# Kernel optimization log

Measured on AMD Instinct MI355X. Metric: run time of the kernel, lower is better.

Reference implementation:

```python
import jax, jax.numpy as jnp
import numpy as np

STRIDE = (1, 1)
PAD = (1, 1)
DIL = (1, 1)
GROUPS = 1
DG = 1  # deformable_groups
KH, KW = 3, 3


def setup_inputs() -> dict:
    key = jax.random.key(0)
    k1, k2, k3, k4 = jax.random.split(key, 4)
    x = jax.random.normal(k1, (8, 256, 64, 64), jnp.float32)
    offset = jax.random.normal(k2, (8, DG * 2 * KH * KW, 64, 64), jnp.float32)
    weight = jax.random.normal(k3, (256, 256, KH, KW), jnp.float32) * 0.05
    bias = jax.random.normal(k4, (256,), jnp.float32)
    return {"x": x, "offset": offset, "weight": weight, "bias": bias}


def _deform_conv2d(x, offset, weight, bias):
    N, C, H, W = x.shape
    Cout = weight.shape[0]
    Ho = (H + 2 * PAD[0] - (DIL[0] * (KH - 1) + 1)) // STRIDE[0] + 1
    Wo = (W + 2 * PAD[1] - (DIL[1] * (KW - 1) + 1)) // STRIDE[1] + 1
    K = KH * KW
    Cg = C // DG

    # offset layout: [N, DG, K, 2(y,x), Ho, Wo]
    off = offset.reshape(N, DG, K, 2, Ho, Wo)

    ky, kx = jnp.meshgrid(jnp.arange(KH), jnp.arange(KW), indexing="ij")
    ky = (ky.reshape(K) * DIL[0]).astype(jnp.float32)  # [K]
    kx = (kx.reshape(K) * DIL[1]).astype(jnp.float32)
    base_y = (jnp.arange(Ho) * STRIDE[0] - PAD[0]).astype(jnp.float32)  # [Ho]
    base_x = (jnp.arange(Wo) * STRIDE[1] - PAD[1]).astype(jnp.float32)  # [Wo]

    # sampling positions [N, DG, K, Ho, Wo]
    py = base_y[None, None, None, :, None] + ky[None, None, :, None, None] + off[:, :, :, 0]
    px = base_x[None, None, None, None, :] + kx[None, None, :, None, None] + off[:, :, :, 1]

    y0f = jnp.floor(py)
    x0f = jnp.floor(px)
    ly = py - y0f
    lx = px - x0f
    hy = 1.0 - ly
    hx = 1.0 - lx
    y0 = y0f.astype(jnp.int32)
    x0 = x0f.astype(jnp.int32)
    y1 = y0 + 1
    x1 = x0 + 1

    img = x.reshape(N, DG, Cg, H * W)

    def gather(yi, xi):
        valid = ((yi >= 0) & (yi < H) & (xi >= 0) & (xi < W)).astype(x.dtype)
        idx = jnp.clip(yi, 0, H - 1) * W + jnp.clip(xi, 0, W - 1)  # [N,DG,K,Ho,Wo]
        flat = idx.reshape(N, DG, 1, K * Ho * Wo)
        v = jnp.take_along_axis(img, flat, axis=3).reshape(N, DG, Cg, K, Ho, Wo)
        return v * valid[:, :, None]

    # bilinear combine -> columns [N, DG, Cg, K, Ho, Wo]
    cols = (
        (hy * hx)[:, :, None] * gather(y0, x0)
        + (hy * lx)[:, :, None] * gather(y0, x1)
        + (ly * hx)[:, :, None] * gather(y1, x0)
        + (ly * lx)[:, :, None] * gather(y1, x1)
    )

    # grouped conv accumulation
    P = Ho * Wo
    cols = cols.reshape(N, GROUPS, C // GROUPS, K, P)
    w = weight.reshape(GROUPS, Cout // GROUPS, C // GROUPS, K)
    out = jnp.einsum("ngckp,gock->ngop", cols, w).reshape(N, Cout, Ho, Wo)
    return out + bias[None, :, None, None]


def reference(x, offset, weight, bias):
    return _deform_conv2d(x, offset, weight, bias)
```

## Files before the change

kernel.cpp:

```cpp
#include <hip/hip_runtime.h>


#define H 64
#define W 64
#define CIN 256
#define COUT 256
#define NIMG 8
#define KTAPS 9
#define CK (CIN * KTAPS)
#define NCHUNK 72

typedef _Float16 f16;
typedef __attribute__((ext_vector_type(8))) _Float16 f16x8;
typedef __attribute__((ext_vector_type(4))) float f32x4;

__global__ __launch_bounds__(256) void dcn_wprep(const float* __restrict__ w,
                                                 f16* __restrict__ wt) {
    __shared__ f16 tw[CK];
    const int co = blockIdx.x;
    const int t = threadIdx.x;
    const float* wr = w + (size_t)co * CK + t * 9;
    float v[9];
#pragma unroll
    for (int j = 0; j < 9; ++j) v[j] = wr[j];
#pragma unroll
    for (int j = 0; j < 9; ++j) tw[j * 256 + t] = (f16)v[j];
    __syncthreads();
    f16* o = wt + (size_t)co * CK;
    for (int i = t; i < CK / 8; i += 256)
        *(f16x8*)(o + i * 8) = *(const f16x8*)(tw + i * 8);
}

__global__ __launch_bounds__(256) void dcn_xprep(const float* __restrict__ x,
                                                 f16* __restrict__ xt) {
    __shared__ f16 tl[64][66];
    const int b = blockIdx.x;
    const int n = b >> 8, pb = (b >> 2) & 63, cb = b & 3;
    const float* xn = x + (size_t)(n * CIN + cb * 64) * (H * W) + pb * 64;
    const int t = threadIdx.x;
    const int c = t >> 4;
    const int p4 = (t & 15) * 4;
#pragma unroll
    for (int pass = 0; pass < 4; ++pass) {
        float4 v = *(const float4*)(xn + (size_t)(c + pass * 16) * (H * W) + p4);
        const int cc = c + pass * 16;
        tl[p4 + 0][cc] = (f16)v.x;
        tl[p4 + 1][cc] = (f16)v.y;
        tl[p4 + 2][cc] = (f16)v.z;
        tl[p4 + 3][cc] = (f16)v.w;
    }
    __syncthreads();
    const int p = t >> 2, cq = (t & 3) * 16;
    f16* dst = xt + (size_t)n * (H * W) * CIN + (size_t)(pb * 64 + p) * CIN + cb * 64 + cq;
    *(f16x8*)dst = *(const f16x8*)&tl[p][cq];
    *(f16x8*)(dst + 8) = *(const f16x8*)&tl[p][cq + 8];
}

__global__ __launch_bounds__(256, 2) void dcn_mfma(
    const f16* __restrict__ xt, const float* __restrict__ offset,
    const f16* __restrict__ wt, const float* __restrict__ bias,
    float* __restrict__ out) {
    __shared__ int s_pix[4][KTAPS][64];
    __shared__ f16 s_wbh[4][KTAPS][64];
    __shared__ f16 s_cols[2][64][40];

    const int tid = threadIdx.x;
    const int bx = blockIdx.x;
    const int n = bx >> 6, t_img = bx & 63;
    const int tile_y = (t_img >> 3) << 3, tile_x = (t_img & 7) << 3;

    const float* offn = offset + (size_t)n * 18 * (H * W);
    for (int e = tid; e < KTAPS * 64; e += 256) {
        int k = e >> 6, p = e & 63;
        int oy = tile_y + (p >> 3), ox = tile_x + (p & 7);
        float offy = offn[(k * 2 + 0) * (H * W) + oy * W + ox];
        float offx = offn[(k * 2 + 1) * (H * W) + oy * W + ox];
        float py = (float)(oy - 1 + (k / 3)) + offy;
        float px = (float)(ox - 1 + (k % 3)) + offx;
        float y0f = floorf(py), x0f = floorf(px);
        int y0 = (int)y0f, x0 = (int)x0f, y1 = y0 + 1, x1 = x0 + 1;
        float ly = py - y0f, lx = px - x0f, hy = 1.f - ly, hx = 1.f - lx;
        bool vy0 = (y0 >= 0) && (y0 < H), vy1 = (y1 >= 0) && (y1 < H);
        bool vx0 = (x0 >= 0) && (x0 < W), vx1 = (x1 >= 0) && (x1 < W);
        int cy0 = min(max(y0, 0), H - 1), cx0 = min(max(x0, 0), W - 1);
        int cy1 = min(max(y1, 0), H - 1), cx1 = min(max(x1, 0), W - 1);
        s_pix[0][k][p] = (cy0 * W + cx0) * (CIN * 2);
        s_pix[1][k][p] = (cy0 * W + cx1) * (CIN * 2);
        s_pix[2][k][p] = (cy1 * W + cx0) * (CIN * 2);
        s_pix[3][k][p] = (cy1 * W + cx1) * (CIN * 2);
        s_wbh[0][k][p] = (f16)((vy0 && vx0) ? hy * hx : 0.f);
        s_wbh[1][k][p] = (f16)((vy0 && vx1) ? hy * lx : 0.f);
        s_wbh[2][k][p] = (f16)((vy1 && vx0) ? ly * hx : 0.f);
        s_wbh[3][k][p] = (f16)((vy1 && vx1) ? ly * lx : 0.f);
    }

    f32x4 acc[4][4];
#pragma unroll
    for (int i = 0; i < 4; ++i)
#pragma unroll
        for (int j = 0; j < 4; ++j) acc[i][j] = (f32x4)0.f;

    const int lane = tid & 63, wv = tid >> 6;
    const int co_base = wv * 64;
    const int pix_s = wv * 16 + (lane >> 2);
    const int cq16 = (lane & 3) * 16;
    const char* xb = (const char*)(xt + (size_t)n * (H * W) * CIN);

    const f16* arow[4];
#pragma unroll
    for (int cf = 0; cf < 4; ++cf)
        arow[cf] = wt + (size_t)(co_base + 16 * cf + (lane & 15)) * CK + (lane >> 4) * 8;

    __syncthreads();

    f16x8 af[4];
    {
        const char* base = xb + cq16;
        f16x8 h0 = *(const f16x8*)(base + s_pix[0][0][pix_s]);
        f16x8 h1 = *(const f16x8*)(base + s_pix[1][0][pix_s]);
        f16x8 h2 = *(const f16x8*)(base + s_pix[2][0][pix_s]);
        f16x8 h3 = *(const f16x8*)(base + s_pix[3][0][pix_s]);
#pragma unroll
        for (int cf = 0; cf < 4; ++cf) af[cf] = *(const f16x8*)(arow[cf]);
        f16x8 v = h0 * s_wbh[0][0][pix_s] + h1 * s_wbh[1][0][pix_s] +
                  h2 * s_wbh[2][0][pix_s] + h3 * s_wbh[3][0][pix_s];
        *(f16x8*)((char*)&s_cols[0][pix_s][0] + cq16) = v;
    }
    __syncthreads();

    for (int cc = 0; cc < NCHUNK; ++cc) {
        const int cur = cc & 1, nx = cur ^ 1;
        const int c1 = cc + 1;
        f16x8 h0, h1, h2, h3, afn[4];
        f16 w0, w1, w2, w3;
        if (c1 < NCHUNK) {
            const int tap = c1 >> 3;
            const char* base = xb + (c1 & 7) * 64 + cq16;
            h0 = *(const f16x8*)(base + s_pix[0][tap][pix_s]);
            h1 = *(const f16x8*)(base + s_pix[1][tap][pix_s]);
            h2 = *(const f16x8*)(base + s_pix[2][tap][pix_s]);
            h3 = *(const f16x8*)(base + s_pix[3][tap][pix_s]);
            w0 = s_wbh[0][tap][pix_s];
            w1 = s_wbh[1][tap][pix_s];
            w2 = s_wbh[2][tap][pix_s];
            w3 = s_wbh[3][tap][pix_s];
            const int k0 = c1 * 32;
#pragma unroll
            for (int cf = 0; cf < 4; ++cf) afn[cf] = *(const f16x8*)(arow[cf] + k0);
        }
        f16x8 bf[4];
#pragma unroll
        for (int pf = 0; pf < 4; ++pf)
            bf[pf] = *(const f16x8*)&s_cols[cur][16 * pf + (lane & 15)][(lane >> 4) * 8];
#pragma unroll
        for (int cf = 0; cf < 4; ++cf)
#pragma unroll
            for (int pf = 0; pf < 4; ++pf)
                acc[cf][pf] =
                    __builtin_amdgcn_mfma_f32_16x16x32_f16(af[cf], bf[pf], acc[cf][pf], 0, 0, 0);
        if (c1 < NCHUNK) {
            f16x8 v = h0 * w0 + h1 * w1 + h2 * w2 + h3 * w3;
            *(f16x8*)((char*)&s_cols[nx][pix_s][0] + cq16) = v;
#pragma unroll
            for (int cf = 0; cf < 4; ++cf) af[cf] = afn[cf];
        }
        __syncthreads();
    }

    float* outn = out + (size_t)n * COUT * (H * W);
#pragma unroll
    for (int cf = 0; cf < 4; ++cf) {
#pragma unroll
        for (int r = 0; r < 4; ++r) {
            int co = co_base + 16 * cf + ((lane >> 4) << 2) + r;
            float b = bias[co];
#pragma unroll
            for (int pf = 0; pf < 4; ++pf) {
                int pp = 16 * pf + (lane & 15);
                int oy = tile_y + (pp >> 3), ox = tile_x + (pp & 7);
                outn[(size_t)co * (H * W) + oy * W + ox] = acc[cf][pf][r] + b;
            }
        }
    }
}

__global__ __launch_bounds__(256) void dcn_transpose_w(const float* __restrict__ w,
                                                       float* __restrict__ wt) {
    __shared__ float tile[32][33];
    const int ckb = blockIdx.x * 32;
    const int cob = blockIdx.y * 32;
    const int tx = threadIdx.x & 31;
    const int ty = threadIdx.x >> 5;
#pragma unroll
    for (int i = 0; i < 32; i += 8)
        tile[ty + i][tx] = w[(size_t)(cob + ty + i) * CK + ckb + tx];
    __syncthreads();
#pragma unroll
    for (int i = 0; i < 32; i += 8)
        wt[(size_t)(ckb + ty + i) * COUT + cob + tx] = tile[tx][ty + i];
}

__global__ __launch_bounds__(256, 2) void dcn_main(
    const float* __restrict__ x, const float* __restrict__ offset,
    const float* __restrict__ wt, const float* __restrict__ bias,
    float* __restrict__ out) {
    __shared__ int s_idx[4][KTAPS][64];
    __shared__ float s_bw[4][KTAPS][64];
    __shared__ float s_W[36][COUT];
    __shared__ float s_cols[36][64];

    const int tid = threadIdx.x;
    const int bx = blockIdx.x;
    const int n = bx >> 6;
    const int t_img = bx & 63;
    const int tile_y = (t_img >> 3) << 3;
    const int tile_x = (t_img & 7) << 3;

    const float* offn = offset + (size_t)n * 18 * (H * W);
    for (int e = tid; e < KTAPS * 64; e += 256) {
        int k = e >> 6, p = e & 63;
        int oy = tile_y + (p >> 3), ox = tile_x + (p & 7);
        float offy = offn[(k * 2 + 0) * (H * W) + oy * W + ox];
        float offx = offn[(k * 2 + 1) * (H * W) + oy * W + ox];
        float py = (float)(oy - 1 + (k / 3)) + offy;
        float px = (float)(ox - 1 + (k % 3)) + offx;
        float y0f = floorf(py), x0f = floorf(px);
        int y0 = (int)y0f, x0 = (int)x0f, y1 = y0 + 1, x1 = x0 + 1;
        float ly = py - y0f, lx = px - x0f, hy = 1.f - ly, hx = 1.f - lx;
        bool vy0 = (y0 >= 0) && (y0 < H), vy1 = (y1 >= 0) && (y1 < H);
        bool vx0 = (x0 >= 0) && (x0 < W), vx1 = (x1 >= 0) && (x1 < W);
        int cy0 = min(max(y0, 0), H - 1), cx0 = min(max(x0, 0), W - 1);
        int cy1 = min(max(y1, 0), H - 1), cx1 = min(max(x1, 0), W - 1);
        s_idx[0][k][p] = cy0 * W + cx0;
        s_idx[1][k][p] = cy0 * W + cx1;
        s_idx[2][k][p] = cy1 * W + cx0;
        s_idx[3][k][p] = cy1 * W + cx1;
        s_bw[0][k][p] = (vy0 && vx0) ? hy * hx : 0.f;
        s_bw[1][k][p] = (vy0 && vx1) ? hy * lx : 0.f;
        s_bw[2][k][p] = (vy1 && vx0) ? ly * hx : 0.f;
        s_bw[3][k][p] = (vy1 && vx1) ? ly * lx : 0.f;
    }

    float acc[8][8];
#pragma unroll
    for (int i = 0; i < 8; ++i)
#pragma unroll
        for (int j = 0; j < 8; ++j) acc[i][j] = 0.f;

    const int ty = tid >> 3;
    const int tx = tid & 7;
    const int q = tid >> 6;
    const int pl = tid & 63;
    const float* xn = x + (size_t)(n * CIN) * (H * W);

    for (int ch = 0; ch < CIN / 4; ++ch) {
        const int c0 = ch * 4;
        __syncthreads();
        {
            const int rbase = q * KTAPS;
            const int co4 = (tid & 63) * 4;
#pragma unroll
            for (int i = 0; i < KTAPS; ++i) {
                int r = rbase + i;
                *reinterpret_cast<float4*>(&s_W[r][co4]) =
                    *reinterpret_cast<const float4*>(&wt[(size_t)(c0 * KTAPS + r) * COUT + co4]);
            }
        }
#pragma unroll
        for (int s = 0; s < KTAPS; ++s) {
            int r = q + 4 * s;
            int c = r / 9;
            int k = r - c * 9;
            const float* xc = xn + (size_t)(c0 + c) * (H * W);
            float v = s_bw[0][k][pl] * xc[s_idx[0][k][pl]] +
                      s_bw[1][k][pl] * xc[s_idx[1][k][pl]] +
                      s_bw[2][k][pl] * xc[s_idx[2][k][pl]] +
                      s_bw[3][k][pl] * xc[s_idx[3][k][pl]];
            s_cols[r][pl] = v;
        }
        __syncthreads();
#pragma unroll 4
        for (int r = 0; r < 36; ++r) {
            const float4 cv0 = *reinterpret_cast<const float4*>(&s_cols[r][tx * 8]);
            const float4 cv1 = *reinterpret_cast<const float4*>(&s_cols[r][tx * 8 + 4]);
            const float4 wv0 = *reinterpret_cast<const float4*>(&s_W[r][ty * 8]);
            const float4 wv1 = *reinterpret_cast<const float4*>(&s_W[r][ty * 8 + 4]);
            const float wa[8] = {wv0.x, wv0.y, wv0.z, wv0.w, wv1.x, wv1.y, wv1.z, wv1.w};
            const float ca[8] = {cv0.x, cv0.y, cv0.z, cv0.w, cv1.x, cv1.y, cv1.z, cv1.w};
#pragma unroll
            for (int i = 0; i < 8; ++i)
#pragma unroll
                for (int j = 0; j < 8; ++j) acc[i][j] += wa[i] * ca[j];
        }
    }

    float* outn = out + (size_t)(n * COUT) * (H * W);
    const int obase = (tile_y + tx) * W + tile_x;
#pragma unroll
    for (int i = 0; i < 8; ++i) {
        int co = ty * 8 + i;
        float b = bias[co];
        float4 o0, o1;
        o0.x = acc[i][0] + b; o0.y = acc[i][1] + b; o0.z = acc[i][2] + b; o0.w = acc[i][3] + b;
        o1.x = acc[i][4] + b; o1.y = acc[i][5] + b; o1.z = acc[i][6] + b; o1.w = acc[i][7] + b;
        float* po = &outn[(size_t)co * (H * W) + obase];
        *reinterpret_cast<float4*>(po) = o0;
        *reinterpret_cast<float4*>(po + 4) = o1;
    }
}

extern "C" void kernel_launch(void* const* d_in, const int* in_sizes, int n_in,
                              void* d_out, int out_size, void* d_ws, size_t ws_size,
                              hipStream_t stream) {
    const float* x = (const float*)d_in[0];
    const float* offset = (const float*)d_in[1];
    const float* weight = (const float*)d_in[2];
    const float* bias = (const float*)d_in[3];
    float* out = (float*)d_out;

    const size_t XT_OFF = 2u * 1024 * 1024;
    const size_t need = XT_OFF + (size_t)NIMG * H * W * CIN * sizeof(f16);

    if (ws_size >= need) {
        f16* wt = (f16*)d_ws;
        f16* xt = (f16*)((char*)d_ws + XT_OFF);
        dcn_wprep<<<COUT, 256, 0, stream>>>(weight, wt);
        dcn_xprep<<<NIMG * 64 * 4, 256, 0, stream>>>(x, xt);
        dcn_mfma<<<NIMG * 64, 256, 0, stream>>>(xt, offset, wt, bias, out);
    } else {
        float* wt = (float*)d_ws;
        dim3 tgrid(CK / 32, COUT / 32);
        dcn_transpose_w<<<tgrid, 256, 0, stream>>>(weight, wt);
        dcn_main<<<NIMG * 64, 256, 0, stream>>>(x, offset, wt, bias, out);
    }
}
```

Measured before the change: 185.7 us.

## Double waves per MFMA block, prefetch gathers two chunks ahead, fuse prep kernels

Merges the weight and input prep kernels into a single launch. The main MFMA kernel moves to 512 threads, so each wave covers 32 pixels instead of 64, and each thread gathers half as much data (f16x4). Bilinear gathers are now issued two chunks ahead to hide global latency. Block-to-image mapping is interleaved across images. The per-wave B-fragment reuse is halved in exchange for more waves per CU to hide gather latency; the occupancy hint of 4 blocks of 512 threads may not be reachable given register pressure.

```diff
diff --git a/kernel.cpp b/kernel.cpp
--- a/kernel.cpp
+++ b/kernel.cpp
@@ -11,52 +11,53 @@
 #define NCHUNK 72
 
 typedef _Float16 f16;
+typedef __attribute__((ext_vector_type(4))) _Float16 f16x4;
 typedef __attribute__((ext_vector_type(8))) _Float16 f16x8;
 typedef __attribute__((ext_vector_type(4))) float f32x4;
 
-__global__ __launch_bounds__(256) void dcn_wprep(const float* __restrict__ w,
-                                                 f16* __restrict__ wt) {
+__global__ __launch_bounds__(256) void dcn_prep(const float* __restrict__ x,
+                                                const float* __restrict__ w,
+                                                f16* __restrict__ xt,
+                                                f16* __restrict__ wt) {
+    __shared__ f16 tl[64][66];
     __shared__ f16 tw[CK];
-    const int co = blockIdx.x;
+    const int b = blockIdx.x;
     const int t = threadIdx.x;
-    const float* wr = w + (size_t)co * CK + t * 9;
-    float v[9];
-#pragma unroll
-    for (int j = 0; j < 9; ++j) v[j] = wr[j];
-#pragma unroll
-    for (int j = 0; j < 9; ++j) tw[j * 256 + t] = (f16)v[j];
-    __syncthreads();
-    f16* o = wt + (size_t)co * CK;
-    for (int i = t; i < CK / 8; i += 256)
-        *(f16x8*)(o + i * 8) = *(const f16x8*)(tw + i * 8);
-}
-
-__global__ __launch_bounds__(256) void dcn_xprep(const float* __restrict__ x,
-                                                 f16* __restrict__ xt) {
-    __shared__ f16 tl[64][66];
-    const int b = blockIdx.x;
-    const int n = b >> 8, pb = (b >> 2) & 63, cb = b & 3;
-    const float* xn = x + (size_t)(n * CIN + cb * 64) * (H * W) + pb * 64;
-    const int t = threadIdx.x;
-    const int c = t >> 4;
-    const int p4 = (t & 15) * 4;
-#pragma unroll
-    for (int pass = 0; pass < 4; ++pass) {
-        float4 v = *(const float4*)(xn + (size_t)(c + pass * 16) * (H * W) + p4);
-        const int cc = c + pass * 16;
-        tl[p4 + 0][cc] = (f16)v.x;
-        tl[p4 + 1][cc] = (f16)v.y;
-        tl[p4 + 2][cc] = (f16)v.z;
-        tl[p4 + 3][cc] = (f16)v.w;
-    }
-    __syncthreads();
-    const int p = t >> 2, cq = (t & 3) * 16;
-    f16* dst = xt + (size_t)n * (H * W) * CIN + (size_t)(pb * 64 + p) * CIN + cb * 64 + cq;
-    *(f16x8*)dst = *(const f16x8*)&tl[p][cq];
-    *(f16x8*)(dst + 8) = *(const f16x8*)&tl[p][cq + 8];
-}
-
-__global__ __launch_bounds__(256, 2) void dcn_mfma(
+    if (b < 2048) {
+        const int n = b >> 8, pb = (b >> 2) & 63, cb = b & 3;
+        const float* xn = x + (size_t)(n * CIN + cb * 64) * (H * W) + pb * 64;
+        const int c = t >> 4;
+        const int p4 = (t & 15) * 4;
+#pragma unroll
+        for (int pass = 0; pass < 4; ++pass) {
+            float4 v = *(const float4*)(xn + (size_t)(c + pass * 16) * (H * W) + p4);
+            const int cc = c + pass * 16;
+            tl[p4 + 0][cc] = (f16)v.x;
+            tl[p4 + 1][cc] = (f16)v.y;
+            tl[p4 + 2][cc] = (f16)v.z;
+            tl[p4 + 3][cc] = (f16)v.w;
+        }
+        __syncthreads();
+        const int p = t >> 2, cq = (t & 3) * 16;
+        f16* dst = xt + (size_t)n * (H * W) * CIN + (size_t)(pb * 64 + p) * CIN + cb * 64 + cq;
+        *(f16x8*)dst = *(const f16x8*)&tl[p][cq];
+        *(f16x8*)(dst + 8) = *(const f16x8*)&tl[p][cq + 8];
+    } else {
+        const int co = b - 2048;
+        const float* wr = w + (size_t)co * CK + t * 9;
+        float v[9];
+#pragma unroll
+        for (int j = 0; j < 9; ++j) v[j] = wr[j];
+#pragma unroll
+        for (int j = 0; j < 9; ++j) tw[j * 256 + t] = (f16)v[j];
+        __syncthreads();
+        f16* o = wt + (size_t)co * CK;
+        for (int i = t; i < CK / 8; i += 256)
+            *(f16x8*)(o + i * 8) = *(const f16x8*)(tw + i * 8);
+    }
+}
+
+__global__ __launch_bounds__(512, 4) void dcn_mfma(
     const f16* __restrict__ xt, const float* __restrict__ offset,
     const f16* __restrict__ wt, const float* __restrict__ bias,
     float* __restrict__ out) {
@@ -66,11 +67,12 @@
 
     const int tid = threadIdx.x;
     const int bx = blockIdx.x;
-    const int n = bx >> 6, t_img = bx & 63;
+    const int n = bx & 7;
+    const int t_img = bx >> 3;
     const int tile_y = (t_img >> 3) << 3, tile_x = (t_img & 7) << 3;
 
     const float* offn = offset + (size_t)n * 18 * (H * W);
-    for (int e = tid; e < KTAPS * 64; e += 256) {
+    for (int e = tid; e < KTAPS * 64; e += 512) {
         int k = e >> 6, p = e & 63;
         int oy = tile_y + (p >> 3), ox = tile_x + (p & 7);
         float offy = offn[(k * 2 + 0) * (H * W) + oy * W + ox];
@@ -94,16 +96,19 @@
         s_wbh[3][k][p] = (f16)((vy1 && vx1) ? ly * lx : 0.f);
     }
 
-    f32x4 acc[4][4];
+    f32x4 acc[4][2];
 #pragma unroll
     for (int i = 0; i < 4; ++i)
 #pragma unroll
-        for (int j = 0; j < 4; ++j) acc[i][j] = (f32x4)0.f;
+        for (int j = 0; j < 2; ++j) acc[i][j] = (f32x4)0.f;
 
     const int lane = tid & 63, wv = tid >> 6;
-    const int co_base = wv * 64;
-    const int pix_s = wv * 16 + (lane >> 2);
-    const int cq16 = (lane & 3) * 16;
+    const int wvco = wv & 3, hp = wv >> 2;
+    const int co_base = wvco * 64;
+    const int pxbase = hp * 32;
+
+    const int pix_g = tid >> 3;
+    const int poff = (tid & 7) * 8;
     const char* xb = (const char*)(xt + (size_t)n * (H * W) * CIN);
 
     const f16* arow[4];
@@ -113,54 +118,63 @@
 
     __syncthreads();
 
+    {
+        const char* base = xb + poff;
+        f16x4 g0 = *(const f16x4*)(base + s_pix[0][0][pix_g]);
+        f16x4 g1 = *(const f16x4*)(base + s_pix[1][0][pix_g]);
+        f16x4 g2 = *(const f16x4*)(base + s_pix[2][0][pix_g]);
+        f16x4 g3 = *(const f16x4*)(base + s_pix[3][0][pix_g]);
+        f16x4 v = g0 * s_wbh[0][0][pix_g] + g1 * s_wbh[1][0][pix_g] +
+                  g2 * s_wbh[2][0][pix_g] + g3 * s_wbh[3][0][pix_g];
+        *(f16x4*)((char*)&s_cols[0][pix_g][0] + poff) = v;
+    }
+    f16x4 hb0, hb1, hb2, hb3;
+    {
+        const char* base = xb + 64 + poff;
+        hb0 = *(const f16x4*)(base + s_pix[0][0][pix_g]);
+        hb1 = *(const f16x4*)(base + s_pix[1][0][pix_g]);
+        hb2 = *(const f16x4*)(base + s_pix[2][0][pix_g]);
+        hb3 = *(const f16x4*)(base + s_pix[3][0][pix_g]);
+    }
     f16x8 af[4];
-    {
-        const char* base = xb + cq16;
-        f16x8 h0 = *(const f16x8*)(base + s_pix[0][0][pix_s]);
-        f16x8 h1 = *(const f16x8*)(base + s_pix[1][0][pix_s]);
-        f16x8 h2 = *(const f16x8*)(base + s_pix[2][0][pix_s]);
-        f16x8 h3 = *(const f16x8*)(base + s_pix[3][0][pix_s]);
-#pragma unroll
-        for (int cf = 0; cf < 4; ++cf) af[cf] = *(const f16x8*)(arow[cf]);
-        f16x8 v = h0 * s_wbh[0][0][pix_s] + h1 * s_wbh[1][0][pix_s] +
-                  h2 * s_wbh[2][0][pix_s] + h3 * s_wbh[3][0][pix_s];
-        *(f16x8*)((char*)&s_cols[0][pix_s][0] + cq16) = v;
-    }
+#pragma unroll
+    for (int cf = 0; cf < 4; ++cf) af[cf] = *(const f16x8*)(arow[cf]);
     __syncthreads();
 
     for (int cc = 0; cc < NCHUNK; ++cc) {
-        const int cur = cc & 1, nx = cur ^ 1;
-        const int c1 = cc + 1;
-        f16x8 h0, h1, h2, h3, afn[4];
-        f16 w0, w1, w2, w3;
+        const int cur = cc & 1;
+        const int c1 = cc + 1, c2i = cc + 2;
         if (c1 < NCHUNK) {
-            const int tap = c1 >> 3;
-            const char* base = xb + (c1 & 7) * 64 + cq16;
-            h0 = *(const f16x8*)(base + s_pix[0][tap][pix_s]);
-            h1 = *(const f16x8*)(base + s_pix[1][tap][pix_s]);
-            h2 = *(const f16x8*)(base + s_pix[2][tap][pix_s]);
-            h3 = *(const f16x8*)(base + s_pix[3][tap][pix_s]);
-            w0 = s_wbh[0][tap][pix_s];
-            w1 = s_wbh[1][tap][pix_s];
-            w2 = s_wbh[2][tap][pix_s];
-            w3 = s_wbh[3][tap][pix_s];
+            const int tap1 = c1 >> 3;
+            f16x4 v = hb0 * s_wbh[0][tap1][pix_g] + hb1 * s_wbh[1][tap1][pix_g] +
+                      hb2 * s_wbh[2][tap1][pix_g] + hb3 * s_wbh[3][tap1][pix_g];
+            *(f16x4*)((char*)&s_cols[cur ^ 1][pix_g][0] + poff) = v;
+        }
+        if (c2i < NCHUNK) {
+            const int tap2 = c2i >> 3;
+            const char* base = xb + (c2i & 7) * 64 + poff;
+            hb0 = *(const f16x4*)(base + s_pix[0][tap2][pix_g]);
+            hb1 = *(const f16x4*)(base + s_pix[1][tap2][pix_g]);
+            hb2 = *(const f16x4*)(base + s_pix[2][tap2][pix_g]);
+            hb3 = *(const f16x4*)(base + s_pix[3][tap2][pix_g]);
+        }
+        f16x8 afn[4];
+        if (c1 < NCHUNK) {
             const int k0 = c1 * 32;
 #pragma unroll
             for (int cf = 0; cf < 4; ++cf) afn[cf] = *(const f16x8*)(arow[cf] + k0);
         }
-        f16x8 bf[4];
-#pragma unroll
-        for (int pf = 0; pf < 4; ++pf)
-            bf[pf] = *(const f16x8*)&s_cols[cur][16 * pf + (lane & 15)][(lane >> 4) * 8];
+        f16x8 bf[2];
+#pragma unroll
+        for (int pf = 0; pf < 2; ++pf)
+            bf[pf] = *(const f16x8*)&s_cols[cur][pxbase + 16 * pf + (lane & 15)][(lane >> 4) * 8];
 #pragma unroll
         for (int cf = 0; cf < 4; ++cf)
 #pragma unroll
-            for (int pf = 0; pf < 4; ++pf)
+            for (int pf = 0; pf < 2; ++pf)
                 acc[cf][pf] =
                     __builtin_amdgcn_mfma_f32_16x16x32_f16(af[cf], bf[pf], acc[cf][pf], 0, 0, 0);
         if (c1 < NCHUNK) {
-            f16x8 v = h0 * w0 + h1 * w1 + h2 * w2 + h3 * w3;
-            *(f16x8*)((char*)&s_cols[nx][pix_s][0] + cq16) = v;
 #pragma unroll
             for (int cf = 0; cf < 4; ++cf) af[cf] = afn[cf];
         }
@@ -175,8 +189,8 @@
             int co = co_base + 16 * cf + ((lane >> 4) << 2) + r;
             float b = bias[co];
 #pragma unroll
-            for (int pf = 0; pf < 4; ++pf) {
-                int pp = 16 * pf + (lane & 15);
+            for (int pf = 0; pf < 2; ++pf) {
+                int pp = pxbase + 16 * pf + (lane & 15);
                 int oy = tile_y + (pp >> 3), ox = tile_x + (pp & 7);
                 outn[(size_t)co * (H * W) + oy * W + ox] = acc[cf][pf][r] + b;
             }
@@ -324,13 +338,12 @@
     if (ws_size >= need) {
         f16* wt = (f16*)d_ws;
         f16* xt = (f16*)((char*)d_ws + XT_OFF);
-        dcn_wprep<<<COUT, 256, 0, stream>>>(weight, wt);
-        dcn_xprep<<<NIMG * 64 * 4, 256, 0, stream>>>(x, xt);
-        dcn_mfma<<<NIMG * 64, 256, 0, stream>>>(xt, offset, wt, bias, out);
+        dcn_prep<<<2048 + COUT, 256, 0, stream>>>(x, weight, xt, wt);
+        dcn_mfma<<<NIMG * 64, 512, 0, stream>>>(xt, offset, wt, bias, out);
     } else {
-        float* wt = (float*)d_ws;
+        float* wtf = (float*)d_ws;
         dim3 tgrid(CK / 32, COUT / 32);
-        dcn_transpose_w<<<tgrid, 256, 0, stream>>>(weight, wt);
-        dcn_main<<<NIMG * 64, 256, 0, stream>>>(x, offset, wt, bias, out);
-    }
-}
+        dcn_transpose_w<<<tgrid, 256, 0, stream>>>(weight, wtf);
+        dcn_main<<<NIMG * 64, 256, 0, stream>>>(x, offset, wtf, bias, out);
+    }
+}
```

Result: slower. 253.8 us (+36.7%).
